# Kernel optimization log

Measured on AMD Instinct MI355X. Metric: run time of the kernel, lower is better.

## Reference

```python
import jax, jax.numpy as jnp
import numpy as np

WS = 8        # window_size
NH = 8        # num_heads
LN_EPS = 1e-5

# static relative-position index table [WS*WS, WS*WS], values in [0, (2*WS-1)**2)
def _rel_index(ws):
    coords = np.arange(ws)
    grid = np.stack(np.meshgrid(coords, coords, indexing='ij')).reshape(2, -1)  # [2, W2]
    rel = grid[:, :, None] - grid[:, None, :]            # [2, W2, W2]
    rel = rel.transpose(1, 2, 0).copy()                   # [W2, W2, 2]
    rel[..., 0] += ws - 1
    rel[..., 1] += ws - 1
    rel[..., 0] *= 2 * ws - 1
    return rel.sum(-1)                                    # [W2, W2]

REL_IDX = jnp.asarray(_rel_index(WS))


def _ln(x):
    # LayerNorm without affine params (elementwise_affine=False)
    mu = jnp.mean(x, axis=-1, keepdims=True)
    var = jnp.var(x, axis=-1, keepdims=True)
    return (x - mu) * jax.lax.rsqrt(var + LN_EPS)


def setup_inputs() -> dict:
    key = jax.random.key(0)
    ks = jax.random.split(key, 16)
    B, Hg, Wg, C = 8, 64, 64, 256
    L = Hg * Wg
    s = 0.02
    inp = {
        'x': jax.random.normal(ks[0], (B, L, C), jnp.float32),
        't_embed': jax.random.normal(ks[1], (B, C), jnp.float32),
        'H': Hg,
        'W': Wg,
        'adaln1_w': s * jax.random.normal(ks[2], (C, 2 * C), jnp.float32),
        'adaln1_b': jnp.zeros((2 * C,), jnp.float32),
        'adaln2_w': s * jax.random.normal(ks[3], (C, 2 * C), jnp.float32),
        'adaln2_b': jnp.zeros((2 * C,), jnp.float32),
        'bias_table': s * jax.random.normal(ks[4], ((2 * WS - 1) ** 2, NH), jnp.float32),
        'q_w': s * jax.random.normal(ks[5], (C, C), jnp.float32),
        'q_b': jnp.zeros((C,), jnp.float32),
        'k_w': s * jax.random.normal(ks[6], (C, C), jnp.float32),
        'k_b': jnp.zeros((C,), jnp.float32),
        'v_w': s * jax.random.normal(ks[7], (C, C), jnp.float32),
        'v_b': jnp.zeros((C,), jnp.float32),
        'o_w': s * jax.random.normal(ks[8], (C, C), jnp.float32),
        'o_b': jnp.zeros((C,), jnp.float32),
        'ffn1_w': s * jax.random.normal(ks[9], (C, 4 * C), jnp.float32),
        'ffn1_b': jnp.zeros((4 * C,), jnp.float32),
        'ffn2_w': s * jax.random.normal(ks[10], (4 * C, C), jnp.float32),
        'ffn2_b': jnp.zeros((C,), jnp.float32),
    }
    return inp


def reference(x, t_embed, H, W, adaln1_w, adaln1_b, adaln2_w, adaln2_b,
              bias_table, q_w, q_b, k_w, k_b, v_w, v_b, o_w, o_b,
              ffn1_w, ffn1_b, ffn2_w, ffn2_b):
    B, L, C = x.shape
    d = C // NH
    W2 = WS * WS
    sh = WS // 2  # cyclic shift (shifted=True)

    # --- AdaLN1 ---
    ss = t_embed @ adaln1_w + adaln1_b              # [B, 2C]
    scale, shift = jnp.split(ss, 2, axis=-1)
    xn = _ln(x) * (1.0 + scale[:, None, :]) + shift[:, None, :]

    # --- shifted window partition ---
    xg = xn.reshape(B, H, W, C)
    xg = jnp.roll(xg, (-sh, -sh), axis=(1, 2))
    xw = xg.reshape(B, H // WS, WS, W // WS, WS, C).transpose(0, 1, 3, 2, 4, 5)
    xw = xw.reshape(-1, W2, C)                       # [nwB, W2, C]
    nwB = xw.shape[0]

    # --- window attention with relative position bias ---
    q = (xw @ q_w + q_b).reshape(nwB, W2, NH, d).transpose(0, 2, 1, 3)
    k = (xw @ k_w + k_b).reshape(nwB, W2, NH, d).transpose(0, 2, 1, 3)
    v = (xw @ v_w + v_b).reshape(nwB, W2, NH, d).transpose(0, 2, 1, 3)
    logits = jnp.einsum('whqd,whkd->whqk', q, k) * (d ** -0.5)
    bias = bias_table[REL_IDX.reshape(-1)].reshape(W2, W2, NH).transpose(2, 0, 1)
    logits = logits + bias[None].astype(logits.dtype)
    attn = jax.nn.softmax(logits, axis=-1)
    out = jnp.einsum('whqk,whkd->whqd', attn, v).transpose(0, 2, 1, 3).reshape(nwB, W2, C)
    out = out @ o_w + o_b

    # --- window reverse + unshift ---
    xm = out.reshape(B, H // WS, W // WS, WS, WS, C).transpose(0, 1, 3, 2, 4, 5)
    xm = xm.reshape(B, H, W, C)
    xm = jnp.roll(xm, (sh, sh), axis=(1, 2))
    x = x + xm.reshape(B, L, C)

    # --- AdaLN2 + FFN (GELU exact, matching torch nn.GELU) ---
    ss2 = t_embed @ adaln2_w + adaln2_b
    sc2, sh2 = jnp.split(ss2, 2, axis=-1)
    xn2 = _ln(x) * (1.0 + sc2[:, None, :]) + sh2[:, None, :]
    h = jax.nn.gelu(xn2 @ ffn1_w + ffn1_b, approximate=False)
    x = x + (h @ ffn2_w + ffn2_b)
    return x
```

## Files before the change

### kernel.cpp

```cpp
#include <hip/hip_runtime.h>
#include <math.h>

#define WS_ 8
#define NH_ 8
#define C_ 256
#define B_ 8
#define M_ 32768
#define SH_ 4
#define LN_EPS 1e-5f
#define SL_ 8388608

typedef __attribute__((ext_vector_type(8))) short bf16x8;
typedef __attribute__((ext_vector_type(4))) float f32x4;

__device__ inline float b2f(unsigned short u) {
    union { unsigned int i; float f; } c; c.i = ((unsigned int)u) << 16; return c.f;
}
__device__ inline unsigned short f2b(float f) {
    union { unsigned int i; float f; } c; c.f = f;
    unsigned int u = c.i;
    return (unsigned short)((u + 0x7FFFu + ((u >> 16) & 1u)) >> 16);
}
__device__ inline float gelu_f(float x) {
    float t = 1.59576912160573f * (x + 0.044715f * x * x * x);
    return x / (1.f + __expf(-t));
}

__global__ void prep_k(const float* __restrict__ qw, const float* __restrict__ kw,
                       const float* __restrict__ vw, const float* __restrict__ ow,
                       const float* __restrict__ f1w, const float* __restrict__ f2w,
                       const float* __restrict__ qb, const float* __restrict__ kb,
                       const float* __restrict__ vb, const float* __restrict__ bt,
                       const float* __restrict__ te,
                       const float* __restrict__ a1w, const float* __restrict__ a1b,
                       const float* __restrict__ a2w, const float* __restrict__ a2b,
                       unsigned short* __restrict__ qkvT, unsigned short* __restrict__ oT,
                       unsigned short* __restrict__ f1T, unsigned short* __restrict__ f2T,
                       float* __restrict__ qkvB, float* __restrict__ bias_full,
                       float* __restrict__ ss1, float* __restrict__ ss2) {
    int t = blockIdx.x * 256 + threadIdx.x;
    if (t < 196608) {
        int n = t >> 8, k = t & 255;
        const float* w = n < 256 ? qw : (n < 512 ? kw : vw);
        qkvT[t] = f2b(w[k * 256 + (n & 255)]);
    } else if (t < 262144) {
        int i = t - 196608; int n = i >> 8, k = i & 255;
        oT[i] = f2b(ow[k * 256 + n]);
    } else if (t < 524288) {
        int i = t - 262144; int n = i >> 8, k = i & 255;
        f1T[i] = f2b(f1w[k * 1024 + n]);
    } else if (t < 786432) {
        int i = t - 524288; int n = i >> 10, k = i & 1023;
        f2T[i] = f2b(f2w[k * 256 + n]);
    } else if (t < 787200) {
        int i = t - 786432;
        qkvB[i] = i < 256 ? qb[i] : (i < 512 ? kb[i - 256] : vb[i - 512]);
    } else if (t < 819968) {
        int i = t - 787200;
        int head = i >> 12, qk = i & 4095;
        int q = qk >> 6, k = qk & 63;
        int qh = q >> 3, qw2 = q & 7, kh = k >> 3, kw2 = k & 7;
        bias_full[i] = bt[((qh - kh + 7) * 15 + (qw2 - kw2 + 7)) * 8 + head];
    } else if (t < 828160) {
        int i = t - 819968;
        int which = i >> 12;
        int rem = i & 4095;
        int b = rem >> 9, col = rem & 511;
        const float* w = which ? a2w : a1w;
        const float* bb = which ? a2b : a1b;
        const float* tr = te + b * C_;
        float acc = bb[col];
        for (int k = 0; k < C_; ++k) acc += tr[k] * w[k * 512 + col];
        (which ? ss2 : ss1)[b * 512 + col] = acc;
    }
}

__global__ __launch_bounds__(256) void ln_win_k(const float* __restrict__ x,
                                                const float* __restrict__ ss,
                                                unsigned short* __restrict__ xw) {
    int t = blockIdx.x * 4 + (threadIdx.x >> 6);
    int lane = threadIdx.x & 63;
    int b = t >> 12, rem = t & 4095;
    int hg = rem >> 6, wg = rem & 63;
    int hs = (hg + SH_) & 63, wsrc = (wg + SH_) & 63;
    size_t src = ((size_t)b << 12) + (hs << 6) + wsrc;
    float4 v = *(const float4*)&x[src * C_ + lane * 4];
    float s = v.x + v.y + v.z + v.w;
    float s2 = v.x * v.x + v.y * v.y + v.z * v.z + v.w * v.w;
#pragma unroll
    for (int m = 1; m < 64; m <<= 1) { s += __shfl_xor(s, m); s2 += __shfl_xor(s2, m); }
    float mu = s * (1.f / 256.f);
    float rstd = rsqrtf(s2 * (1.f / 256.f) - mu * mu + LN_EPS);
    float4 sc = *(const float4*)&ss[b * 512 + lane * 4];
    float4 sh = *(const float4*)&ss[b * 512 + 256 + lane * 4];
    int win = (b << 6) + ((hg >> 3) << 3) + (wg >> 3);
    int pos = ((hg & 7) << 3) + (wg & 7);
    ushort4 pk;
    pk.x = f2b((v.x - mu) * rstd * (1.f + sc.x) + sh.x);
    pk.y = f2b((v.y - mu) * rstd * (1.f + sc.y) + sh.y);
    pk.z = f2b((v.z - mu) * rstd * (1.f + sc.z) + sh.z);
    pk.w = f2b((v.w - mu) * rstd * (1.f + sc.w) + sh.w);
    *(ushort4*)(xw + (size_t)(win * 64 + pos) * C_ + lane * 4) = pk;
}

__global__ __launch_bounds__(256) void ln_k(const float* __restrict__ x,
                                            const float* __restrict__ ss,
                                            unsigned short* __restrict__ y_out) {
    int t = blockIdx.x * 4 + (threadIdx.x >> 6);
    int lane = threadIdx.x & 63;
    int b = t >> 12;
    float4 v = *(const float4*)&x[(size_t)t * C_ + lane * 4];
    float s = v.x + v.y + v.z + v.w;
    float s2 = v.x * v.x + v.y * v.y + v.z * v.z + v.w * v.w;
#pragma unroll
    for (int m = 1; m < 64; m <<= 1) { s += __shfl_xor(s, m); s2 += __shfl_xor(s2, m); }
    float mu = s * (1.f / 256.f);
    float rstd = rsqrtf(s2 * (1.f / 256.f) - mu * mu + LN_EPS);
    float4 sc = *(const float4*)&ss[b * 512 + lane * 4];
    float4 sh = *(const float4*)&ss[b * 512 + 256 + lane * 4];
    ushort4 pk;
    pk.x = f2b((v.x - mu) * rstd * (1.f + sc.x) + sh.x);
    pk.y = f2b((v.y - mu) * rstd * (1.f + sc.y) + sh.y);
    pk.z = f2b((v.z - mu) * rstd * (1.f + sc.z) + sh.z);
    pk.w = f2b((v.w - mu) * rstd * (1.f + sc.w) + sh.w);
    *(ushort4*)(y_out + (size_t)t * C_ + lane * 4) = pk;
}

template <int KDIM, int MODE, int NT, int MINW>
__global__ __launch_bounds__(256, MINW) void gemm_bf16_k(
    const unsigned short* __restrict__ A, const unsigned short* __restrict__ Bt,
    const float* __restrict__ bias, const float* __restrict__ res,
    void* __restrict__ Cout, int Nout) {
    __shared__ __align__(16) unsigned short As[2][128 * 32];
    __shared__ __align__(16) unsigned short Bs[2][128 * 32];
    const int blk = blockIdx.x;
    const int xcd = blk & 7;
    const int idx = blk >> 3;
    const int mt = xcd + ((idx / NT) << 3);
    const int nt = idx % NT;
    const int bm = mt * 128, bn = nt * 128;
    const int tid = threadIdx.x;
    const int w = tid >> 6, lane = tid & 63;
    const int quad = lane >> 4, l16 = lane & 15;
    const int wm = (w >> 1) * 64, wn = (w & 1) * 64;
    const int srow = lane >> 2;
    const int qlog = ((lane & 3) ^ ((lane >> 3) & 3)) << 3;
    const int rsw = ((l16 >> 1) & 3) << 3;

    f32x4 acc[4][4] = {};

    for (int k0 = 0; k0 < KDIM; k0 += 64) {
        if (k0) __syncthreads();
#pragma unroll
        for (int h = 0; h < 2; ++h) {
#pragma unroll
            for (int j = 0; j < 2; ++j) {
                int r = j * 64 + w * 16 + srow;
                const unsigned short* ga = A + (size_t)(bm + r) * KDIM + k0 + h * 32 + qlog;
                unsigned short* la = &As[h][j * 2048 + w * 512 + lane * 8];
                __builtin_amdgcn_global_load_lds(
                    (const __attribute__((address_space(1))) void*)ga,
                    (__attribute__((address_space(3))) void*)la, 16, 0, 0);
                const unsigned short* gb = Bt + (size_t)(bn + r) * KDIM + k0 + h * 32 + qlog;
                unsigned short* lb = &Bs[h][j * 2048 + w * 512 + lane * 8];
                __builtin_amdgcn_global_load_lds(
                    (const __attribute__((address_space(1))) void*)gb,
                    (__attribute__((address_space(3))) void*)lb, 16, 0, 0);
            }
        }
        __syncthreads();
#pragma unroll
        for (int h = 0; h < 2; ++h) {
            bf16x8 af[4], bfr[4];
#pragma unroll
            for (int i = 0; i < 4; ++i)
                af[i] = *(const bf16x8*)&As[h][(wm + i * 16 + l16) * 32 + ((quad << 3) ^ rsw)];
#pragma unroll
            for (int j = 0; j < 4; ++j)
                bfr[j] = *(const bf16x8*)&Bs[h][(wn + j * 16 + l16) * 32 + ((quad << 3) ^ rsw)];
#pragma unroll
            for (int i = 0; i < 4; ++i)
#pragma unroll
                for (int j = 0; j < 4; ++j)
                    acc[i][j] = __builtin_amdgcn_mfma_f32_16x16x32_bf16(
                        bfr[j], af[i], acc[i][j], 0, 0, 0);
        }
    }

#pragma unroll
    for (int i = 0; i < 4; ++i) {
        const int row = bm + wm + i * 16 + l16;
        size_t rowbase = 0;
        if (MODE == 0) {
            int win = row >> 6, pos = row & 63;
            rowbase = (size_t)win * 16384 + pos * 32;
        } else if (MODE == 1) {
            int win = row >> 6, pos = row & 63;
            int b = win >> 6, wh = (win >> 3) & 7, ww = win & 7;
            int hg = (wh << 3) + (pos >> 3), wg = (ww << 3) + (pos & 7);
            int hd = (hg + SH_) & 63, wd = (wg + SH_) & 63;
            rowbase = (((size_t)b << 12) + (hd << 6) + wd) * C_;
        } else {
            rowbase = (size_t)row * Nout;
        }
#pragma unroll
        for (int j = 0; j < 4; ++j) {
            const int col = bn + wn + j * 16 + quad * 4;
            float4 bv = *(const float4*)&bias[col];
            float v0 = acc[i][j][0] + bv.x, v1 = acc[i][j][1] + bv.y;
            float v2 = acc[i][j][2] + bv.z, v3 = acc[i][j][3] + bv.w;
            if (MODE == 0) {
                int which = col >> 8, head = (col >> 5) & 7, dc = col & 31;
                ushort4 pk = {f2b(v0), f2b(v1), f2b(v2), f2b(v3)};
                *(ushort4*)((unsigned short*)Cout + (size_t)which * SL_ + rowbase +
                            head * 2048 + dc) = pk;
            } else if (MODE == 1) {
                float4 rv = *(const float4*)&res[rowbase + col];
                float4 ov = {v0 + rv.x, v1 + rv.y, v2 + rv.z, v3 + rv.w};
                *(float4*)&((float*)Cout)[rowbase + col] = ov;
            } else if (MODE == 2) {
                ushort4 pk = {f2b(gelu_f(v0)), f2b(gelu_f(v1)),
                              f2b(gelu_f(v2)), f2b(gelu_f(v3))};
                *(ushort4*)((unsigned short*)Cout + rowbase + col) = pk;
            } else {
                float4 rv = *(const float4*)&res[rowbase + col];
                float4 ov = {v0 + rv.x, v1 + rv.y, v2 + rv.z, v3 + rv.w};
                *(float4*)&((float*)Cout)[rowbase + col] = ov;
            }
        }
    }
}

__global__ __launch_bounds__(256) void attn_mfma_k(
    const unsigned short* __restrict__ qkv, const float* __restrict__ bias_full,
    unsigned short* __restrict__ attn_out) {
    __shared__ __align__(16) unsigned short Pb[4][64 * 66];
    __shared__ __align__(16) unsigned short Vt[4][32 * 66];
    const int w = threadIdx.x >> 6, lane = threadIdx.x & 63;
    const int wh = blockIdx.x * 4 + w;
    const int win = wh >> 3, head = wh & 7;
    const int quad = lane >> 4, l16 = lane & 15;

    const unsigned short* qp = qkv + (size_t)win * 16384 + head * 2048;
    const unsigned short* kp = qp + SL_;
    const unsigned short* vp = qp + 2 * (size_t)SL_;

    {
        const uint4* v4 = (const uint4*)(vp + lane * 32);
        unsigned short* dst = &Vt[w][0];
#pragma unroll
        for (int c = 0; c < 4; ++c) {
            uint4 u = v4[c];
            unsigned int uu[4] = {u.x, u.y, u.z, u.w};
#pragma unroll
            for (int p = 0; p < 4; ++p) {
                int d0 = c * 8 + p * 2;
                dst[d0 * 66 + lane] = (unsigned short)(uu[p] & 0xffff);
                dst[(d0 + 1) * 66 + lane] = (unsigned short)(uu[p] >> 16);
            }
        }
    }

    bf16x8 qf[4], kf[4];
#pragma unroll
    for (int i = 0; i < 4; ++i) {
        qf[i] = *(const bf16x8*)(qp + (i * 16 + l16) * 32 + quad * 8);
        kf[i] = *(const bf16x8*)(kp + (i * 16 + l16) * 32 + quad * 8);
    }

    f32x4 s[4][4] = {};
#pragma unroll
    for (int i = 0; i < 4; ++i)
#pragma unroll
        for (int j = 0; j < 4; ++j)
            s[i][j] = __builtin_amdgcn_mfma_f32_16x16x32_bf16(qf[i], kf[j], s[i][j], 0, 0, 0);

    const float scale = 0.17677669529663687f;
    const float* bf = bias_full + head * 4096;
    float rs[4][4];
#pragma unroll
    for (int i = 0; i < 4; ++i) {
#pragma unroll
        for (int r = 0; r < 4; ++r) {
            int row = i * 16 + quad * 4 + r;
            float acc = 0.f;
#pragma unroll
            for (int j = 0; j < 4; ++j) {
                float e = __expf(s[i][j][r] * scale + bf[row * 64 + j * 16 + l16]);
                s[i][j][r] = e;
                acc += e;
            }
#pragma unroll
            for (int msk = 1; msk < 16; msk <<= 1) acc += __shfl_xor(acc, msk);
            rs[i][r] = 1.f / acc;
        }
    }

#pragma unroll
    for (int i = 0; i < 4; ++i)
#pragma unroll
        for (int j = 0; j < 4; ++j)
#pragma unroll
            for (int r = 0; r < 4; ++r)
                Pb[w][(i * 16 + quad * 4 + r) * 66 + j * 16 + l16] = f2b(s[i][j][r]);

    __syncthreads();

    f32x4 o[4][2] = {};
#pragma unroll
    for (int st = 0; st < 2; ++st) {
        bf16x8 bv[2];
#pragma unroll
        for (int jo = 0; jo < 2; ++jo)
            bv[jo] = *(const bf16x8*)&Vt[w][(jo * 16 + l16) * 66 + st * 32 + quad * 8];
#pragma unroll
        for (int i = 0; i < 4; ++i) {
            bf16x8 af = *(const bf16x8*)&Pb[w][(i * 16 + l16) * 66 + st * 32 + quad * 8];
#pragma unroll
            for (int jo = 0; jo < 2; ++jo)
                o[i][jo] = __builtin_amdgcn_mfma_f32_16x16x32_bf16(af, bv[jo], o[i][jo], 0, 0, 0);
        }
    }

#pragma unroll
    for (int i = 0; i < 4; ++i)
#pragma unroll
        for (int jo = 0; jo < 2; ++jo)
#pragma unroll
            for (int r = 0; r < 4; ++r) {
                int row = i * 16 + quad * 4 + r;
                int d = jo * 16 + l16;
                attn_out[((size_t)(win * 64 + row)) * C_ + head * 32 + d] =
                    f2b(o[i][jo][r] * rs[i][r]);
            }
}

extern "C" void kernel_launch(void* const* d_in, const int* in_sizes, int n_in,
                              void* d_out, int out_size, void* d_ws, size_t ws_size,
                              hipStream_t stream) {
    const float* x        = (const float*)d_in[0];
    const float* t_embed  = (const float*)d_in[1];
    const float* adaln1_w = (const float*)d_in[4];
    const float* adaln1_b = (const float*)d_in[5];
    const float* adaln2_w = (const float*)d_in[6];
    const float* adaln2_b = (const float*)d_in[7];
    const float* bt       = (const float*)d_in[8];
    const float* q_w = (const float*)d_in[9],  *q_b = (const float*)d_in[10];
    const float* k_w = (const float*)d_in[11], *k_b = (const float*)d_in[12];
    const float* v_w = (const float*)d_in[13], *v_b = (const float*)d_in[14];
    const float* o_w = (const float*)d_in[15], *o_b = (const float*)d_in[16];
    const float* f1_w = (const float*)d_in[17], *f1_b = (const float*)d_in[18];
    const float* f2_w = (const float*)d_in[19], *f2_b = (const float*)d_in[20];
    float* out = (float*)d_out;

    char* wsb = (char*)d_ws;
    float* ss1            = (float*)(wsb + 0);
    float* ss2            = (float*)(wsb + 16384);
    float* qkvB           = (float*)(wsb + 32768);
    unsigned short* qkvT  = (unsigned short*)(wsb + 36864);
    unsigned short* oT    = (unsigned short*)(wsb + 430080);
    unsigned short* f1T   = (unsigned short*)(wsb + 561152);
    unsigned short* f2T   = (unsigned short*)(wsb + 1085440);
    float* bias_full      = (float*)(wsb + 1609728);
    unsigned short* xw    = (unsigned short*)(wsb + 2097152);
    unsigned short* qkv   = (unsigned short*)(wsb + 18874368);
    unsigned short* attn  = (unsigned short*)(wsb + 69206016);
    unsigned short* xn2   = xw;
    unsigned short* hbuf  = qkv;
    float* x1             = (float*)(wsb + 85983232);

    prep_k<<<3235, 256, 0, stream>>>(q_w, k_w, v_w, o_w, f1_w, f2_w, q_b, k_b, v_b, bt,
                                     t_embed, adaln1_w, adaln1_b, adaln2_w, adaln2_b,
                                     qkvT, oT, f1T, f2T, qkvB, bias_full, ss1, ss2);
    ln_win_k<<<8192, 256, 0, stream>>>(x, ss1, xw);

    gemm_bf16_k<256, 0, 6, 3><<<1536, 256, 0, stream>>>(xw, qkvT, qkvB, nullptr, qkv, 768);

    attn_mfma_k<<<1024, 256, 0, stream>>>(qkv, bias_full, attn);

    gemm_bf16_k<256, 1, 2, 1><<<512, 256, 0, stream>>>(attn, oT, o_b, x, x1, 256);
    ln_k<<<8192, 256, 0, stream>>>(x1, ss2, xn2);
    gemm_bf16_k<256, 2, 8, 3><<<2048, 256, 0, stream>>>(xn2, f1T, f1_b, nullptr, hbuf, 1024);
    gemm_bf16_k<1024, 3, 2, 1><<<512, 256, 0, stream>>>(hbuf, f2T, f2_b, x1, out, 256);
}
```

Baseline: 267.3 us.

## Replace GEMM with 8-wave larger-tile kernel using 4-stage async LDS pipeline

Replaces the 256-thread 128x128 double-buffered GEMM with a 512-thread kernel that uses 128x256 or 256x256 tiles and a 4-deep ring of LDS buffers. Global-to-LDS loads are issued three K-steps ahead and gated with explicit vmcnt waits and raw barriers. MFMA sections are raised in priority with setprio. This is meant to hide global load latency and improve data reuse per block, at the cost of fewer blocks per GEMM (possibly under-filling CUs), more LDS per block and high register pressure from 8xNJ accumulators.

Measured after the change: 286.8 us. 7.3% more time.

```diff
diff --git a/kernel.cpp b/kernel.cpp
--- a/kernel.cpp
+++ b/kernel.cpp
@@ -24,6 +24,19 @@
 __device__ inline float gelu_f(float x) {
     float t = 1.59576912160573f * (x + 0.044715f * x * x * x);
     return x / (1.f + __expf(-t));
+}
+
+template <int N> __device__ __forceinline__ void wait_vm() {
+    if constexpr (N == 0)       asm volatile("s_waitcnt vmcnt(0)" ::: "memory");
+    else if constexpr (N == 3)  asm volatile("s_waitcnt vmcnt(3)" ::: "memory");
+    else if constexpr (N == 4)  asm volatile("s_waitcnt vmcnt(4)" ::: "memory");
+    else if constexpr (N == 6)  asm volatile("s_waitcnt vmcnt(6)" ::: "memory");
+    else if constexpr (N == 8)  asm volatile("s_waitcnt vmcnt(8)" ::: "memory");
+    else if constexpr (N == 9)  asm volatile("s_waitcnt vmcnt(9)" ::: "memory");
+    else                        asm volatile("s_waitcnt vmcnt(12)" ::: "memory");
+}
+__device__ __forceinline__ void bar() {
+    asm volatile("s_barrier" ::: "memory");
 }
 
 __global__ void prep_k(const float* __restrict__ qw, const float* __restrict__ kw,
@@ -126,70 +139,89 @@
     *(ushort4*)(y_out + (size_t)t * C_ + lane * 4) = pk;
 }
 
-template <int KDIM, int MODE, int NT, int MINW>
-__global__ __launch_bounds__(256, MINW) void gemm_bf16_k(
+template <int KDIM, int MODE, int MW, int NJ, int NT>
+__global__ __launch_bounds__(512, 2) void gemm8_k(
     const unsigned short* __restrict__ A, const unsigned short* __restrict__ Bt,
     const float* __restrict__ bias, const float* __restrict__ res,
     void* __restrict__ Cout, int Nout) {
-    __shared__ __align__(16) unsigned short As[2][128 * 32];
-    __shared__ __align__(16) unsigned short Bs[2][128 * 32];
+    constexpr int LOADS = MW + 2;
+    constexpr int NW = 8 / MW;
+    __shared__ __align__(16) unsigned short As[4][MW * 128 * 32];
+    __shared__ __align__(16) unsigned short Bs[4][256 * 32];
+
     const int blk = blockIdx.x;
     const int xcd = blk & 7;
     const int idx = blk >> 3;
     const int mt = xcd + ((idx / NT) << 3);
     const int nt = idx % NT;
-    const int bm = mt * 128, bn = nt * 128;
+    const int bm = mt * (MW * 128), bn = nt * 256;
     const int tid = threadIdx.x;
     const int w = tid >> 6, lane = tid & 63;
     const int quad = lane >> 4, l16 = lane & 15;
-    const int wm = (w >> 1) * 64, wn = (w & 1) * 64;
-    const int srow = lane >> 2;
-    const int qlog = ((lane & 3) ^ ((lane >> 3) & 3)) << 3;
+    const int wrow = (w / NW) * 128;
+    const int wcol = (w % NW) * (NJ * 16);
     const int rsw = ((l16 >> 1) & 3) << 3;
-
-    f32x4 acc[4][4] = {};
-
-    for (int k0 = 0; k0 < KDIM; k0 += 64) {
-        if (k0) __syncthreads();
-#pragma unroll
-        for (int h = 0; h < 2; ++h) {
-#pragma unroll
-            for (int j = 0; j < 2; ++j) {
-                int r = j * 64 + w * 16 + srow;
-                const unsigned short* ga = A + (size_t)(bm + r) * KDIM + k0 + h * 32 + qlog;
-                unsigned short* la = &As[h][j * 2048 + w * 512 + lane * 8];
-                __builtin_amdgcn_global_load_lds(
-                    (const __attribute__((address_space(1))) void*)ga,
-                    (__attribute__((address_space(3))) void*)la, 16, 0, 0);
-                const unsigned short* gb = Bt + (size_t)(bn + r) * KDIM + k0 + h * 32 + qlog;
-                unsigned short* lb = &Bs[h][j * 2048 + w * 512 + lane * 8];
-                __builtin_amdgcn_global_load_lds(
-                    (const __attribute__((address_space(1))) void*)gb,
-                    (__attribute__((address_space(3))) void*)lb, 16, 0, 0);
-            }
-        }
-        __syncthreads();
-#pragma unroll
-        for (int h = 0; h < 2; ++h) {
-            bf16x8 af[4], bfr[4];
-#pragma unroll
-            for (int i = 0; i < 4; ++i)
-                af[i] = *(const bf16x8*)&As[h][(wm + i * 16 + l16) * 32 + ((quad << 3) ^ rsw)];
-#pragma unroll
-            for (int j = 0; j < 4; ++j)
-                bfr[j] = *(const bf16x8*)&Bs[h][(wn + j * 16 + l16) * 32 + ((quad << 3) ^ rsw)];
-#pragma unroll
-            for (int i = 0; i < 4; ++i)
-#pragma unroll
-                for (int j = 0; j < 4; ++j)
-                    acc[i][j] = __builtin_amdgcn_mfma_f32_16x16x32_bf16(
-                        bfr[j], af[i], acc[i][j], 0, 0, 0);
-        }
-    }
-
-#pragma unroll
-    for (int i = 0; i < 4; ++i) {
-        const int row = bm + wm + i * 16 + l16;
+    const int rch = (quad << 3) ^ rsw;
+
+    const int srow = tid >> 2;
+    const int gch = ((tid & 3) ^ ((srow >> 1) & 3)) << 3;
+    const unsigned short* gA = A + (size_t)(bm + srow) * KDIM + gch;
+    const unsigned short* gB = Bt + (size_t)(bn + srow) * KDIM + gch;
+    const int ldst = srow * 32 + (tid & 3) * 8;
+
+    f32x4 acc[8][NJ] = {};
+
+    auto stage = [&](int buf, int k0) {
+#pragma unroll
+        for (int s = 0; s < MW; ++s)
+            __builtin_amdgcn_global_load_lds(
+                (const __attribute__((address_space(1))) void*)(gA + (size_t)s * 128 * KDIM + k0),
+                (__attribute__((address_space(3))) void*)&As[buf][s * 4096 + ldst], 16, 0, 0);
+#pragma unroll
+        for (int s = 0; s < 2; ++s)
+            __builtin_amdgcn_global_load_lds(
+                (const __attribute__((address_space(1))) void*)(gB + (size_t)s * 128 * KDIM + k0),
+                (__attribute__((address_space(3))) void*)&Bs[buf][s * 4096 + ldst], 16, 0, 0);
+    };
+
+    auto compute = [&](int ks) {
+        const unsigned short* as0 = &As[ks & 3][0];
+        const unsigned short* bs0 = &Bs[ks & 3][0];
+        bf16x8 af[8], bfr[NJ];
+#pragma unroll
+        for (int i = 0; i < 8; ++i)
+            af[i] = *(const bf16x8*)&as0[(wrow + i * 16 + l16) * 32 + rch];
+#pragma unroll
+        for (int j = 0; j < NJ; ++j)
+            bfr[j] = *(const bf16x8*)&bs0[(wcol + j * 16 + l16) * 32 + rch];
+        __builtin_amdgcn_s_setprio(1);
+#pragma unroll
+        for (int i = 0; i < 8; ++i)
+#pragma unroll
+            for (int j = 0; j < NJ; ++j)
+                acc[i][j] = __builtin_amdgcn_mfma_f32_16x16x32_bf16(
+                    bfr[j], af[i], acc[i][j], 0, 0, 0);
+        __builtin_amdgcn_s_setprio(0);
+    };
+
+    constexpr int NK = KDIM / 32;
+    static_assert(NK >= 4, "need >=4 K-steps");
+    stage(0, 0); stage(1, 32); stage(2, 64);
+#pragma unroll
+    for (int ks = 0; ks < NK - 3; ++ks) {
+        stage((ks + 3) & 3, (ks + 3) * 32);
+        wait_vm<3 * LOADS>();
+        bar();
+        compute(ks);
+        bar();
+    }
+    wait_vm<2 * LOADS>(); bar(); compute(NK - 3); bar();
+    wait_vm<1 * LOADS>(); bar(); compute(NK - 2); bar();
+    wait_vm<0>();         bar(); compute(NK - 1);
+
+#pragma unroll
+    for (int i = 0; i < 8; ++i) {
+        const int row = bm + wrow + i * 16 + l16;
         size_t rowbase = 0;
         if (MODE == 0) {
             int win = row >> 6, pos = row & 63;
@@ -204,8 +236,8 @@
             rowbase = (size_t)row * Nout;
         }
 #pragma unroll
-        for (int j = 0; j < 4; ++j) {
-            const int col = bn + wn + j * 16 + quad * 4;
+        for (int j = 0; j < NJ; ++j) {
+            const int col = bn + wcol + j * 16 + quad * 4;
             float4 bv = *(const float4*)&bias[col];
             float v0 = acc[i][j][0] + bv.x, v1 = acc[i][j][1] + bv.y;
             float v2 = acc[i][j][2] + bv.z, v3 = acc[i][j][3] + bv.w;
@@ -374,12 +406,12 @@
                                      qkvT, oT, f1T, f2T, qkvB, bias_full, ss1, ss2);
     ln_win_k<<<8192, 256, 0, stream>>>(x, ss1, xw);
 
-    gemm_bf16_k<256, 0, 6, 3><<<1536, 256, 0, stream>>>(xw, qkvT, qkvB, nullptr, qkv, 768);
+    gemm8_k<256, 0, 1, 2, 3><<<768, 512, 0, stream>>>(xw, qkvT, qkvB, nullptr, qkv, 768);
 
     attn_mfma_k<<<1024, 256, 0, stream>>>(qkv, bias_full, attn);
 
-    gemm_bf16_k<256, 1, 2, 1><<<512, 256, 0, stream>>>(attn, oT, o_b, x, x1, 256);
+    gemm8_k<256, 1, 1, 2, 1><<<256, 512, 0, stream>>>(attn, oT, o_b, x, x1, 256);
     ln_k<<<8192, 256, 0, stream>>>(x1, ss2, xn2);
-    gemm_bf16_k<256, 2, 8, 3><<<2048, 256, 0, stream>>>(xn2, f1T, f1_b, nullptr, hbuf, 1024);
-    gemm_bf16_k<1024, 3, 2, 1><<<512, 256, 0, stream>>>(hbuf, f2T, f2_b, x1, out, 256);
-}
+    gemm8_k<256, 2, 2, 4, 4><<<512, 512, 0, stream>>>(xn2, f1T, f1_b, nullptr, hbuf, 1024);
+    gemm8_k<1024, 3, 1, 2, 1><<<256, 512, 0, stream>>>(hbuf, f2T, f2_b, x1, out, 256);
+}
```

## Fuse FFN1+GELU and FFN2 into one kernel keeping hidden tile in LDS

Applied to the files above, without the earlier changes.

Replaces the two FFN GEMM launches with one kernel. Each 512-thread block computes a 64x1024 GELU hidden tile, stores it as bf16 in a 128KB XOR-swizzled LDS buffer, then multiplies it by the second weight matrix and adds bias and residual. This removes the global write and read of the 32768x1024 hidden buffer and one launch. The cost is a very large LDS footprint that limits occupancy, only 512 blocks, and B operands loaded straight from global memory without LDS staging.

New measurement: 300.6 us. +12.5%, slower.

```diff
diff --git a/kernel.cpp b/kernel.cpp
--- a/kernel.cpp
+++ b/kernel.cpp
@@ -231,6 +231,100 @@
     }
 }
 
+__global__ __launch_bounds__(512, 2) void ffn_fused_k(
+    const unsigned short* __restrict__ xn2, const unsigned short* __restrict__ f1T,
+    const unsigned short* __restrict__ f2T, const float* __restrict__ f1b,
+    const float* __restrict__ f2bias, const float* __restrict__ x1,
+    float* __restrict__ out) {
+    __shared__ __align__(16) unsigned short hs[64 * 1024];
+    const int tid = threadIdx.x;
+    const int w = tid >> 6, lane = tid & 63;
+    const int quad = lane >> 4, l16 = lane & 15;
+    const int brow = blockIdx.x * 64;
+
+    {
+        f32x4 acc[4][8] = {};
+        const unsigned short* ap = xn2 + (size_t)(brow + l16) * 256 + quad * 8;
+        const unsigned short* bp = f1T + (size_t)(w * 128 + l16) * 256 + quad * 8;
+#pragma unroll
+        for (int k = 0; k < 8; ++k) {
+            bf16x8 ax[4], bf1[8];
+#pragma unroll
+            for (int i = 0; i < 4; ++i)
+                ax[i] = *(const bf16x8*)(ap + (size_t)i * 16 * 256 + k * 32);
+#pragma unroll
+            for (int j = 0; j < 8; ++j)
+                bf1[j] = *(const bf16x8*)(bp + (size_t)j * 16 * 256 + k * 32);
+            __builtin_amdgcn_s_setprio(1);
+#pragma unroll
+            for (int i = 0; i < 4; ++i)
+#pragma unroll
+                for (int j = 0; j < 8; ++j)
+                    acc[i][j] = __builtin_amdgcn_mfma_f32_16x16x32_bf16(
+                        bf1[j], ax[i], acc[i][j], 0, 0, 0);
+            __builtin_amdgcn_s_setprio(0);
+        }
+#pragma unroll
+        for (int i = 0; i < 4; ++i) {
+            int row = i * 16 + l16;
+#pragma unroll
+            for (int j = 0; j < 8; ++j) {
+                int col = w * 128 + j * 16 + quad * 4;
+                float4 bv = *(const float4*)&f1b[col];
+                ushort4 pk;
+                pk.x = f2b(gelu_f(acc[i][j][0] + bv.x));
+                pk.y = f2b(gelu_f(acc[i][j][1] + bv.y));
+                pk.z = f2b(gelu_f(acc[i][j][2] + bv.z));
+                pk.w = f2b(gelu_f(acc[i][j][3] + bv.w));
+                int c = col >> 3;
+                int half = (col >> 2) & 1;
+                int cs = c ^ (row & 7);
+                *(ushort4*)&hs[row * 1024 + cs * 8 + half * 4] = pk;
+            }
+        }
+    }
+    __syncthreads();
+
+    {
+        f32x4 acc[4][2] = {};
+        const unsigned short* bp = f2T + (size_t)(w * 32 + l16) * 1024 + quad * 8;
+#pragma unroll
+        for (int k = 0; k < 32; ++k) {
+            bf16x8 ah[4], bf2[2];
+#pragma unroll
+            for (int jo = 0; jo < 2; ++jo)
+                bf2[jo] = *(const bf16x8*)(bp + (size_t)jo * 16 * 1024 + k * 32);
+#pragma unroll
+            for (int i = 0; i < 4; ++i) {
+                int row = i * 16 + l16;
+                int c = (k * 4 + quad) ^ (row & 7);
+                ah[i] = *(const bf16x8*)&hs[row * 1024 + c * 8];
+            }
+            __builtin_amdgcn_s_setprio(1);
+#pragma unroll
+            for (int i = 0; i < 4; ++i)
+#pragma unroll
+                for (int jo = 0; jo < 2; ++jo)
+                    acc[i][jo] = __builtin_amdgcn_mfma_f32_16x16x32_bf16(
+                        bf2[jo], ah[i], acc[i][jo], 0, 0, 0);
+            __builtin_amdgcn_s_setprio(0);
+        }
+#pragma unroll
+        for (int i = 0; i < 4; ++i) {
+            int row = brow + i * 16 + l16;
+#pragma unroll
+            for (int jo = 0; jo < 2; ++jo) {
+                int col = w * 32 + jo * 16 + quad * 4;
+                float4 bv = *(const float4*)&f2bias[col];
+                float4 rv = *(const float4*)&x1[(size_t)row * 256 + col];
+                float4 ov = {acc[i][jo][0] + bv.x + rv.x, acc[i][jo][1] + bv.y + rv.y,
+                             acc[i][jo][2] + bv.z + rv.z, acc[i][jo][3] + bv.w + rv.w};
+                *(float4*)&out[(size_t)row * 256 + col] = ov;
+            }
+        }
+    }
+}
+
 __global__ __launch_bounds__(256) void attn_mfma_k(
     const unsigned short* __restrict__ qkv, const float* __restrict__ bias_full,
     unsigned short* __restrict__ attn_out) {
@@ -366,7 +460,6 @@
     unsigned short* qkv   = (unsigned short*)(wsb + 18874368);
     unsigned short* attn  = (unsigned short*)(wsb + 69206016);
     unsigned short* xn2   = xw;
-    unsigned short* hbuf  = qkv;
     float* x1             = (float*)(wsb + 85983232);
 
     prep_k<<<3235, 256, 0, stream>>>(q_w, k_w, v_w, o_w, f1_w, f2_w, q_b, k_b, v_b, bt,
@@ -380,6 +473,6 @@
 
     gemm_bf16_k<256, 1, 2, 1><<<512, 256, 0, stream>>>(attn, oT, o_b, x, x1, 256);
     ln_k<<<8192, 256, 0, stream>>>(x1, ss2, xn2);
-    gemm_bf16_k<256, 2, 8, 3><<<2048, 256, 0, stream>>>(xn2, f1T, f1_b, nullptr, hbuf, 1024);
-    gemm_bf16_k<1024, 3, 2, 1><<<512, 256, 0, stream>>>(hbuf, f2T, f2_b, x1, out, 256);
-}
+
+    ffn_fused_k<<<512, 512, 0, stream>>>(xn2, f1T, f2T, f1_b, f2_b, x1, out);
+}
```
